# Performance work log

Hardware: AMD Instinct MI355X
Metric: run time of the kernel (lower is better)

The kernel has to match this reference:

```python
import jax, jax.numpy as jnp
import numpy as np

INF = 1000000000000.0
HEAD_SIZE = 64
HEADS = 12
MAX_LENGTH = 512


def _rope_tables(dim, max_length):
    inv_freq = 1.0 / (10000.0 ** (jnp.arange(0, dim, 2, dtype=jnp.float32) / dim))
    t = jnp.arange(max_length, dtype=jnp.float32)
    freqs = t[:, None] * inv_freq[None, :]  # [L, dim/2]
    return jnp.sin(freqs), jnp.cos(freqs)


def _apply_rope(t, sin, cos):
    # t: [B, L, d]; sin/cos: [L, d/2]
    t1, t2 = t[..., 0::2], t[..., 1::2]
    out = jnp.stack([t1 * cos - t2 * sin, t1 * sin + t2 * cos], axis=-1)
    return out.reshape(t.shape)


def setup_inputs() -> dict:
    key = jax.random.key(0)
    k1, k2, k3, k4, k5 = jax.random.split(key, 5)
    B, L, H = 16, 512, 1024
    inputs = jax.random.normal(k1, (B, L, H), dtype=jnp.float32)
    attention_mask = jnp.ones((B, L), dtype=jnp.float32)
    s1 = 1.0 / np.sqrt(H)
    s2 = 1.0 / np.sqrt(HEAD_SIZE * 2)
    W1 = jax.random.normal(k2, (H, HEAD_SIZE * 2), dtype=jnp.float32) * s1
    b1 = jax.random.normal(k3, (HEAD_SIZE * 2,), dtype=jnp.float32) * s1
    W2 = jax.random.normal(k4, (HEAD_SIZE * 2, HEADS * 2), dtype=jnp.float32) * s2
    b2 = jax.random.normal(k5, (HEADS * 2,), dtype=jnp.float32) * s2
    return {"inputs": inputs, "attention_mask": attention_mask,
            "W1": W1, "b1": b1, "W2": W2, "b2": b2}


def reference(inputs, attention_mask, W1, b1, W2, b2):
    B, L, _ = inputs.shape
    x = inputs @ W1 + b1                      # [B, L, 2*head_size]
    qw, kw = x[..., 0::2], x[..., 1::2]        # [B, L, head_size] each
    sin, cos = _rope_tables(HEAD_SIZE, MAX_LENGTH)
    sin, cos = sin[:L], cos[:L]
    qw = _apply_rope(qw, sin, cos)
    kw = _apply_rope(kw, sin, cos)
    logits = jnp.einsum('bmd,bnd->bmn', qw, kw) / (HEAD_SIZE ** 0.5)  # [B, L, L]
    bias = jnp.swapaxes(x @ W2 + b2, 1, 2) / 2.0                       # [B, 2*heads, L]
    # logits[b,h,m,n] = score[b,m,n] + bias_even[b,h,n] + bias_odd[b,h,m]
    logits = logits[:, None] + bias[:, 0::2, None, :] + bias[:, 1::2, :, None]
    attn_mask = 1.0 - attention_mask[:, None, None, :] * attention_mask[:, None, :, None]
    logits = logits - attn_mask * INF
    tril = jnp.tril(jnp.ones((L, L), dtype=logits.dtype), k=-1)
    logits = logits - tril * INF
    return logits
```

## Files before the change

kernel.cpp:

```cpp
#include <hip/hip_runtime.h>
#include <hip/hip_bf16.h>

typedef short bf16x8 __attribute__((ext_vector_type(8)));
typedef float f32x4 __attribute__((ext_vector_type(4)));
typedef unsigned short u16;
typedef unsigned short u16x4 __attribute__((ext_vector_type(4)));
typedef unsigned short u16x8 __attribute__((ext_vector_type(8)));

#define FINF 1.0e12f

__device__ __forceinline__ u16 f2b(float f) {
  union { float f; unsigned int u; } x; x.f = f;
  unsigned int r = x.u + 0x7fffu + ((x.u >> 16) & 1u);
  return (u16)(r >> 16);
}

__global__ __launch_bounds__(256) void k0_w1frag(const float* __restrict__ W1,
                                                 u16* __restrict__ w1f) {
  int idx = blockIdx.x * 256 + threadIdx.x;
  int k = idx >> 7, c = idx & 127;
  float v = W1[idx];
  int chunk = k >> 6, kk = k & 63;
  int ks = kk >> 5, km = kk & 31, kg = km >> 3, i = km & 7;
  int nt = c >> 4, ln = c & 15;
  int dst = chunk * 8192 + (nt * 2 + ks) * 512 + (kg * 16 + ln) * 8 + i;
  w1f[dst] = f2b(v);
}

__global__ __launch_bounds__(256) void k1_prep(
    const float* __restrict__ inputs, const u16* __restrict__ w1f,
    const float* __restrict__ b1, const float* __restrict__ W2,
    const float* __restrict__ b2,
    u16* __restrict__ qw, u16* __restrict__ kw,
    float* __restrict__ biasE, float* __restrict__ biasO) {
  __shared__ __align__(16) char smem[49536];
  float* w2t = (float*)(smem + 36864);
  float* xt  = (float*)smem;

  int t = threadIdx.x;
  int lane = t & 63, w = t >> 6;
  int r0 = blockIdx.x * 16;
  int b = r0 >> 9, l0 = r0 & 511;

  #pragma unroll
  for (int i = 0; i < 12; ++i) {
    int idx = t + i * 256;
    int k = idx / 24, c = idx - k * 24;
    w2t[c * 132 + k] = W2[idx];
  }

  f32x4 acc[2];
  acc[0] = (f32x4){0.f, 0.f, 0.f, 0.f};
  acc[1] = (f32x4){0.f, 0.f, 0.f, 0.f};

  int wnt = w * 2;

  int arow_s = t >> 4;
  int aseg = t & 15;
  const float* ain = &inputs[(size_t)(r0 + arow_s) * 1024 + aseg * 4];
  int abyt = (arow_s * 128 + aseg * 8) ^ ((arow_s & 7) << 4);
  const float4* wsrcAll = (const float4*)w1f;

  float4 a0 = *(const float4*)(ain);
  float4 wr0 = wsrcAll[t];
  float4 wr1 = wsrcAll[t + 256];
  float4 wr2 = wsrcAll[t + 512];
  float4 wr3 = wsrcAll[t + 768];
  {
    u16x4 av;
    av[0] = f2b(a0.x); av[1] = f2b(a0.y); av[2] = f2b(a0.z); av[3] = f2b(a0.w);
    *(u16x4*)(smem + abyt) = av;
    float4* wd = (float4*)(smem + 4096);
    wd[t] = wr0; wd[t + 256] = wr1; wd[t + 512] = wr2; wd[t + 768] = wr3;
  }
  __syncthreads();

  for (int ch = 0; ch < 16; ++ch) {
    if (ch < 15) {
      a0 = *(const float4*)(ain + (ch + 1) * 64);
      const float4* wsrc = wsrcAll + (ch + 1) * 1024;
      wr0 = wsrc[t]; wr1 = wsrc[t + 256]; wr2 = wsrc[t + 512]; wr3 = wsrc[t + 768];
    }
    {
      const char* Ab = smem + (ch & 1) * 2048;
      const u16* Wb = (const u16*)(smem + 4096 + (ch & 1) * 16384);
      int arow = lane & 15;
      int hi = lane >> 4;
      #pragma unroll
      for (int ks = 0; ks < 2; ++ks) {
        int cb = ks * 64 + hi * 16;
        bf16x8 a = *(const bf16x8*)(Ab + ((arow * 128 + cb) ^ ((arow & 7) << 4)));
        #pragma unroll
        for (int nti = 0; nti < 2; ++nti) {
          int nt = wnt + nti;
          bf16x8 bb = *(const bf16x8*)&Wb[((nt * 2 + ks) * 64 + lane) * 8];
          acc[nti] = __builtin_amdgcn_mfma_f32_16x16x32_bf16(a, bb, acc[nti], 0, 0, 0);
        }
      }
    }
    if (ch < 15) {
      int q = (ch + 1) & 1;
      u16x4 av;
      av[0] = f2b(a0.x); av[1] = f2b(a0.y); av[2] = f2b(a0.z); av[3] = f2b(a0.w);
      *(u16x4*)(smem + q * 2048 + abyt) = av;
      float4* wd = (float4*)(smem + 4096 + q * 16384);
      wd[t] = wr0; wd[t + 256] = wr1; wd[t + 512] = wr2; wd[t + 768] = wr3;
    }
    __syncthreads();
  }
  __syncthreads();

  #pragma unroll
  for (int nti = 0; nti < 2; ++nti) {
    int c = (wnt + nti) * 16 + (lane & 15);
    float b1v = b1[c];
    #pragma unroll
    for (int r = 0; r < 4; ++r) {
      int row = ((lane >> 4) << 2) + r;
      xt[row * 132 + c] = acc[nti][r] + b1v;
    }
  }
  __syncthreads();

  {
    int r = t >> 4, jb = (t & 15) * 2;
    int l = l0 + r;
    float fl = (float)l;
    u16x4 qv, kv;
    #pragma unroll
    for (int p = 0; p < 2; ++p) {
      int j = jb + p;
      float4 x4 = *(const float4*)&xt[r * 132 + 4 * j];
      float invf = exp2f(-0.4152410118609203f * (float)j);
      float ang = fl * invf;
      float rev = ang * 0.15915494309189535f;
      rev = rev - floorf(rev);
      float sv, cv;
      __sincosf(rev * 6.2831853071795864f, &sv, &cv);
      qv[2 * p] = f2b(x4.x * cv - x4.z * sv);
      qv[2 * p + 1] = f2b(x4.x * sv + x4.z * cv);
      kv[2 * p] = f2b(x4.y * cv - x4.w * sv);
      kv[2 * p + 1] = f2b(x4.y * sv + x4.w * cv);
    }
    size_t base = ((size_t)(b * 512 + l)) * 64 + jb * 2;
    *(u16x4*)&qw[base] = qv;
    *(u16x4*)&kw[base] = kv;
  }

  if (t < 192) {
    int c = t >> 3;
    int rg = (t & 7) * 2;
    float s0 = b2[c], s1 = s0;
    #pragma unroll
    for (int k4 = 0; k4 < 32; ++k4) {
      float4 wv = *(const float4*)&w2t[c * 132 + k4 * 4];
      float4 x0 = *(const float4*)&xt[(rg + 0) * 132 + k4 * 4];
      float4 x1 = *(const float4*)&xt[(rg + 1) * 132 + k4 * 4];
      s0 += x0.x * wv.x + x0.y * wv.y + x0.z * wv.z + x0.w * wv.w;
      s1 += x1.x * wv.x + x1.y * wv.y + x1.z * wv.z + x1.w * wv.w;
    }
    int h = c >> 1;
    size_t o = ((size_t)(b * 12 + h)) * 512 + l0 + rg;
    float2 sv = {s0 * 0.5f, s1 * 0.5f};
    if (c & 1) *(float2*)&biasO[o] = sv;
    else       *(float2*)&biasE[o] = sv;
  }
}

__global__ __launch_bounds__(256) void k2_main(
    const u16* __restrict__ qw, const u16* __restrict__ kw,
    const float* __restrict__ biasE, const float* __restrict__ biasO,
    const float* __restrict__ amask, float* __restrict__ out) {
  __shared__ char smem[24448];
  u16* Q = (u16*)smem;
  u16* K = (u16*)(smem + 8192);
  float* qkL = (float*)smem;
  float* BN = (float*)(smem + 17408);
  float* BM = (float*)(smem + 17408 + 3264);
  float* AMm = (float*)(smem + 17408 + 6528);
  float* AMn = AMm + 64;

  int t = threadIdx.x;
  int lane = t & 63, w = t >> 6;
  int n0 = blockIdx.x * 64, m0 = blockIdx.y * 64, b = blockIdx.z;
  bool skip = (m0 >= n0 + 64);

  if (!skip) {
    int row = t >> 2, sg = t & 3;
    const u16x8* qsrc = (const u16x8*)&qw[((size_t)(b * 512 + m0 + row)) * 64 + sg * 16];
    u16x8 q0 = qsrc[0], q1 = qsrc[1];
    const u16x8* ksrc = (const u16x8*)&kw[((size_t)(b * 512 + n0 + row)) * 64 + sg * 16];
    u16x8 k0v = ksrc[0], k1v = ksrc[1];
    int swz = (row & 7) << 4;
    int byt = row * 128 + sg * 32;
    *(u16x8*)((char*)Q + ((byt) ^ swz)) = q0;
    *(u16x8*)((char*)Q + ((byt + 16) ^ swz)) = q1;
    *(u16x8*)((char*)K + ((byt) ^ swz)) = k0v;
    *(u16x8*)((char*)K + ((byt + 16) ^ swz)) = k1v;
  }
  if (t < 192) {
    int h = t >> 4, kq = t & 15;
    *(float4*)&BN[h * 68 + kq * 4] =
        *(const float4*)&biasE[((size_t)(b * 12 + h)) * 512 + n0 + kq * 4];
    *(float4*)&BM[h * 68 + kq * 4] =
        *(const float4*)&biasO[((size_t)(b * 12 + h)) * 512 + m0 + kq * 4];
  } else if (t < 224) {
    int i = t - 192;
    if (i < 16) *(float4*)&AMm[i * 4] = *(const float4*)&amask[b * 512 + m0 + i * 4];
    else { int ii = i - 16; *(float4*)&AMn[ii * 4] = *(const float4*)&amask[b * 512 + n0 + ii * 4]; }
  }
  __syncthreads();

  if (!skip) {
    f32x4 acc[4];
    #pragma unroll
    for (int nt = 0; nt < 4; ++nt) acc[nt] = (f32x4){0.f, 0.f, 0.f, 0.f};
    int mrow = w * 16 + (lane & 15);
    int hi = lane >> 4;
    #pragma unroll
    for (int ks = 0; ks < 2; ++ks) {
      int cb = ks * 64 + hi * 16;
      bf16x8 a = *(const bf16x8*)((const char*)Q +
                                  ((mrow * 128 + cb) ^ ((mrow & 7) << 4)));
      #pragma unroll
      for (int nt = 0; nt < 4; ++nt) {
        int nr = nt * 16 + (lane & 15);
        bf16x8 bb = *(const bf16x8*)((const char*)K +
                                     ((nr * 128 + cb) ^ ((nr & 7) << 4)));
        acc[nt] = __builtin_amdgcn_mfma_f32_16x16x32_bf16(a, bb, acc[nt], 0, 0, 0);
      }
    }
    __syncthreads();
    #pragma unroll
    for (int nt = 0; nt < 4; ++nt)
      #pragma unroll
      for (int r = 0; r < 4; ++r)
        qkL[(w * 16 + hi * 4 + r) * 68 + nt * 16 + (lane & 15)] = acc[nt][r];
    __syncthreads();
  }

  int a15 = t & 15, mb = t >> 4;
  float amn0 = AMn[a15 * 4 + 0], amn1 = AMn[a15 * 4 + 1];
  float amn2 = AMn[a15 * 4 + 2], amn3 = AMn[a15 * 4 + 3];
  float vals[4][4];
  #pragma unroll
  for (int mi = 0; mi < 4; ++mi) {
    int m = mb + 16 * mi;
    int mg = m0 + m;
    float amm = AMm[m];
    int ng = n0 + a15 * 4;
    float p0 = (1.f - amm * amn0) * FINF + ((mg > ng + 0) ? FINF : 0.f);
    float p1 = (1.f - amm * amn1) * FINF + ((mg > ng + 1) ? FINF : 0.f);
    float p2 = (1.f - amm * amn2) * FINF + ((mg > ng + 2) ? FINF : 0.f);
    float p3 = (1.f - amm * amn3) * FINF + ((mg > ng + 3) ? FINF : 0.f);
    if (!skip) {
      float4 qk = *(const float4*)&qkL[m * 68 + a15 * 4];
      vals[mi][0] = qk.x * 0.125f - p0;
      vals[mi][1] = qk.y * 0.125f - p1;
      vals[mi][2] = qk.z * 0.125f - p2;
      vals[mi][3] = qk.w * 0.125f - p3;
    } else {
      vals[mi][0] = -p0; vals[mi][1] = -p1; vals[mi][2] = -p2; vals[mi][3] = -p3;
    }
  }

  size_t outbase = (size_t)(b * 12) * 262144 + (size_t)m0 * 512 + n0 + a15 * 4;
  #pragma unroll
  for (int h = 0; h < 12; ++h) {
    float4 bn = *(const float4*)&BN[h * 68 + a15 * 4];
    #pragma unroll
    for (int mi = 0; mi < 4; ++mi) {
      int m = mb + 16 * mi;
      float bm = BM[h * 68 + m];
      float4 v;
      v.x = vals[mi][0] + bn.x + bm;
      v.y = vals[mi][1] + bn.y + bm;
      v.z = vals[mi][2] + bn.z + bm;
      v.w = vals[mi][3] + bn.w + bm;
      *(float4*)&out[outbase + (size_t)h * 262144 + (size_t)m * 512] = v;
    }
  }
}

extern "C" void kernel_launch(void* const* d_in, const int* in_sizes, int n_in,
                              void* d_out, int out_size, void* d_ws, size_t ws_size,
                              hipStream_t stream) {
  const float* inputs = (const float*)d_in[0];
  const float* amask  = (const float*)d_in[1];
  const float* W1     = (const float*)d_in[2];
  const float* b1     = (const float*)d_in[3];
  const float* W2     = (const float*)d_in[4];
  const float* b2     = (const float*)d_in[5];
  float* out = (float*)d_out;

  char* ws = (char*)d_ws;
  u16* qw      = (u16*)(ws);
  u16* kw      = (u16*)(ws + (1u << 20));
  float* biasE = (float*)(ws + (2u << 20));
  float* biasO = (float*)(ws + (2u << 20) + 393216u);
  u16* w1f     = (u16*)(ws + (2u << 20) + 786432u);

  k0_w1frag<<<512, 256, 0, stream>>>(W1, w1f);
  k1_prep<<<512, 256, 0, stream>>>(inputs, w1f, b1, W2, b2, qw, kw, biasE, biasO);
  k2_main<<<dim3(8, 8, 16), 256, 0, stream>>>(qw, kw, biasE, biasO, amask, out);
}
```

Baseline: 55.95 us.

## Load W1 fragments straight into registers and preload whole A tile to LDS

The W1 fragment kernel now has each thread produce one 8-element bf16 fragment with a single vector store, launched with fewer blocks. In k1_prep the whole 16x1024 input row tile is converted to bf16 and stored in LDS once up front. Each wave then streams its own W1 MFMA fragments directly from global memory into double-buffered registers, so W1 no longer goes through LDS and the per-chunk __syncthreads barriers are gone. This removes LDS traffic and synchronisation from the GEMM loop, at the cost of more register pressure and an unpipelined upfront input load.

```diff
diff --git a/kernel.cpp b/kernel.cpp
--- a/kernel.cpp
+++ b/kernel.cpp
@@ -17,14 +17,18 @@
 
 __global__ __launch_bounds__(256) void k0_w1frag(const float* __restrict__ W1,
                                                  u16* __restrict__ w1f) {
-  int idx = blockIdx.x * 256 + threadIdx.x;
-  int k = idx >> 7, c = idx & 127;
-  float v = W1[idx];
-  int chunk = k >> 6, kk = k & 63;
-  int ks = kk >> 5, km = kk & 31, kg = km >> 3, i = km & 7;
-  int nt = c >> 4, ln = c & 15;
-  int dst = chunk * 8192 + (nt * 2 + ks) * 512 + (kg * 16 + ln) * 8 + i;
-  w1f[dst] = f2b(v);
+  int t8 = blockIdx.x * 256 + threadIdx.x;
+  int ln = t8 & 15;
+  int kg = (t8 >> 4) & 3;
+  int ksnt = (t8 >> 6) & 15;
+  int chunk = t8 >> 10;
+  int ks = ksnt & 1, nt = ksnt >> 1;
+  int kbase = chunk * 64 + ks * 32 + kg * 8;
+  int c = nt * 16 + ln;
+  u16x8 v;
+  #pragma unroll
+  for (int i = 0; i < 8; ++i) v[i] = f2b(W1[(size_t)(kbase + i) * 128 + c]);
+  *(u16x8*)&w1f[t8 * 8] = v;
 }
 
 __global__ __launch_bounds__(256) void k1_prep(
@@ -33,8 +37,8 @@
     const float* __restrict__ b2,
     u16* __restrict__ qw, u16* __restrict__ kw,
     float* __restrict__ biasE, float* __restrict__ biasO) {
-  __shared__ __align__(16) char smem[49536];
-  float* w2t = (float*)(smem + 36864);
+  __shared__ __align__(16) char smem[45440];
+  float* w2t = (float*)(smem + 32768);
   float* xt  = (float*)smem;
 
   int t = threadIdx.x;
@@ -49,64 +53,57 @@
     w2t[c * 132 + k] = W2[idx];
   }
 
+  {
+    int r = t >> 4, c4 = (t & 15) * 4;
+    const float* src = &inputs[(size_t)(r0 + r) * 1024 + c4];
+    int swz = (r & 7) << 4;
+    int bbase = r * 2048 + c4 * 2;
+    #pragma unroll
+    for (int j = 0; j < 16; ++j) {
+      float4 f = *(const float4*)(src + j * 64);
+      u16x4 v4;
+      v4[0] = f2b(f.x); v4[1] = f2b(f.y); v4[2] = f2b(f.z); v4[3] = f2b(f.w);
+      *(u16x4*)(smem + ((bbase + j * 128) ^ swz)) = v4;
+    }
+  }
+  __syncthreads();
+
   f32x4 acc[2];
   acc[0] = (f32x4){0.f, 0.f, 0.f, 0.f};
   acc[1] = (f32x4){0.f, 0.f, 0.f, 0.f};
-
   int wnt = w * 2;
-
-  int arow_s = t >> 4;
-  int aseg = t & 15;
-  const float* ain = &inputs[(size_t)(r0 + arow_s) * 1024 + aseg * 4];
-  int abyt = (arow_s * 128 + aseg * 8) ^ ((arow_s & 7) << 4);
-  const float4* wsrcAll = (const float4*)w1f;
-
-  float4 a0 = *(const float4*)(ain);
-  float4 wr0 = wsrcAll[t];
-  float4 wr1 = wsrcAll[t + 256];
-  float4 wr2 = wsrcAll[t + 512];
-  float4 wr3 = wsrcAll[t + 768];
-  {
-    u16x4 av;
-    av[0] = f2b(a0.x); av[1] = f2b(a0.y); av[2] = f2b(a0.z); av[3] = f2b(a0.w);
-    *(u16x4*)(smem + abyt) = av;
-    float4* wd = (float4*)(smem + 4096);
-    wd[t] = wr0; wd[t + 256] = wr1; wd[t + 512] = wr2; wd[t + 768] = wr3;
-  }
-  __syncthreads();
-
+  int arow = lane & 15, hi = lane >> 4;
+  int swzr = (arow & 7) << 4;
+  int abase = arow * 2048 + hi * 16;
+  const u16* wbase = w1f + lane * 8 + (size_t)wnt * 1024;
+
+  bf16x8 wf0[4], wf1[4];
+  #pragma unroll
+  for (int q = 0; q < 4; ++q)
+    wf0[q] = *(const bf16x8*)(wbase + q * 512);
+  #pragma unroll
   for (int ch = 0; ch < 16; ++ch) {
     if (ch < 15) {
-      a0 = *(const float4*)(ain + (ch + 1) * 64);
-      const float4* wsrc = wsrcAll + (ch + 1) * 1024;
-      wr0 = wsrc[t]; wr1 = wsrc[t + 256]; wr2 = wsrc[t + 512]; wr3 = wsrc[t + 768];
-    }
-    {
-      const char* Ab = smem + (ch & 1) * 2048;
-      const u16* Wb = (const u16*)(smem + 4096 + (ch & 1) * 16384);
-      int arow = lane & 15;
-      int hi = lane >> 4;
-      #pragma unroll
-      for (int ks = 0; ks < 2; ++ks) {
-        int cb = ks * 64 + hi * 16;
-        bf16x8 a = *(const bf16x8*)(Ab + ((arow * 128 + cb) ^ ((arow & 7) << 4)));
+      const u16* wc = wbase + (ch + 1) * 8192;
+      if (ch & 1) {
         #pragma unroll
-        for (int nti = 0; nti < 2; ++nti) {
-          int nt = wnt + nti;
-          bf16x8 bb = *(const bf16x8*)&Wb[((nt * 2 + ks) * 64 + lane) * 8];
-          acc[nti] = __builtin_amdgcn_mfma_f32_16x16x32_bf16(a, bb, acc[nti], 0, 0, 0);
-        }
+        for (int q = 0; q < 4; ++q) wf0[q] = *(const bf16x8*)(wc + q * 512);
+      } else {
+        #pragma unroll
+        for (int q = 0; q < 4; ++q) wf1[q] = *(const bf16x8*)(wc + q * 512);
       }
     }
-    if (ch < 15) {
-      int q = (ch + 1) & 1;
-      u16x4 av;
-      av[0] = f2b(a0.x); av[1] = f2b(a0.y); av[2] = f2b(a0.z); av[3] = f2b(a0.w);
-      *(u16x4*)(smem + q * 2048 + abyt) = av;
-      float4* wd = (float4*)(smem + 4096 + q * 16384);
-      wd[t] = wr0; wd[t + 256] = wr1; wd[t + 512] = wr2; wd[t + 768] = wr3;
-    }
-    __syncthreads();
+    #pragma unroll
+    for (int ks = 0; ks < 2; ++ks) {
+      bf16x8 a = *(const bf16x8*)(smem + ((abase + ch * 128 + ks * 64) ^ swzr));
+      if (ch & 1) {
+        acc[0] = __builtin_amdgcn_mfma_f32_16x16x32_bf16(a, wf1[ks], acc[0], 0, 0, 0);
+        acc[1] = __builtin_amdgcn_mfma_f32_16x16x32_bf16(a, wf1[2 + ks], acc[1], 0, 0, 0);
+      } else {
+        acc[0] = __builtin_amdgcn_mfma_f32_16x16x32_bf16(a, wf0[ks], acc[0], 0, 0, 0);
+        acc[1] = __builtin_amdgcn_mfma_f32_16x16x32_bf16(a, wf0[2 + ks], acc[1], 0, 0, 0);
+      }
+    }
   }
   __syncthreads();
 
@@ -300,7 +297,7 @@
   float* biasO = (float*)(ws + (2u << 20) + 393216u);
   u16* w1f     = (u16*)(ws + (2u << 20) + 786432u);
 
-  k0_w1frag<<<512, 256, 0, stream>>>(W1, w1f);
+  k0_w1frag<<<64, 256, 0, stream>>>(W1, w1f);
   k1_prep<<<512, 256, 0, stream>>>(inputs, w1f, b1, W2, b2, qw, kw, biasE, biasO);
   k2_main<<<dim3(8, 8, 16), 256, 0, stream>>>(qw, kw, biasE, biasO, amask, out);
 }
```

Result: slower. 57.94 us (+3.5%).
